# Kernel tuning notes

Measured on AMD Instinct MI355X. Metric: run time of the kernel, lower is better.

## Reference

```python
import jax, jax.numpy as jnp
import numpy as np

SEQ, EMBED, H, QLR, KVLR, RD, VD = 4096, 2048, 16, 512, 512, 64, 128
KD = VD + RD  # full key/query head dim (content + rope)


def _make_rotary_pe(seq_len, dim):
    inv_freq = 1.0 / jnp.power(10000.0, jnp.arange(0, dim, 2) / dim)
    t = jnp.arange(seq_len)
    freqs = jnp.outer(t, inv_freq)  # (seq, dim//2)
    return jnp.sin(freqs), jnp.cos(freqs)


def _apply_rope(x, sin, cos):
    # x: (seq, ..., dim); sin/cos: (seq, dim//2)
    d = x.shape[-1] // 2
    x1, x2 = x[..., :d], x[..., d:]
    sin2 = jnp.concatenate([sin, sin], axis=-1)
    cos2 = jnp.concatenate([cos, cos], axis=-1)
    ne = x.ndim - 2
    sin2 = sin2.reshape(sin2.shape[0], *[1] * ne, sin2.shape[1])
    cos2 = cos2.reshape(cos2.shape[0], *[1] * ne, cos2.shape[1])
    rot = jnp.concatenate([-x2, x1], axis=-1)
    return x * cos2 + rot * sin2


def setup_inputs() -> dict:
    key = jax.random.key(0)
    ks = jax.random.split(key, 8)

    def w(k, out_dim, in_dim):
        return jax.random.normal(k, (out_dim, in_dim), dtype=jnp.float32) * (1.0 / np.sqrt(in_dim))

    x = jax.random.normal(ks[0], (SEQ, EMBED), dtype=jnp.float32)
    mask = jnp.tril(jnp.ones((SEQ, SEQ), dtype=bool))  # causal
    return {
        "x": x,
        "mask": mask,
        "w_q_down": w(ks[1], QLR, EMBED),
        "w_q_up": w(ks[2], H * VD, QLR),
        "w_q_rope": w(ks[3], H * RD, QLR),
        "w_kv_down": w(ks[4], KVLR, EMBED),
        "w_kv_up": w(ks[5], H * 2 * VD, KVLR),
        "w_k_rope": w(ks[6], RD, EMBED),
        "w_out": w(ks[7], EMBED, H * VD),
    }


def reference(x, mask, w_q_down, w_q_up, w_q_rope, w_kv_down, w_kv_up, w_k_rope, w_out):
    seq = x.shape[0]
    # query path through low-rank bottleneck
    c_q = x @ w_q_down.T                                   # (S, QLR)
    q_content = (c_q @ w_q_up.T).reshape(seq, H, VD)       # (S, H, VD)
    q_rope = (c_q @ w_q_rope.T).reshape(seq, H, RD)        # (S, H, RD)
    # kv path through shared low-rank bottleneck
    c_kv = x @ w_kv_down.T                                 # (S, KVLR)
    kv = c_kv @ w_kv_up.T                                  # (S, H*2*VD)
    k_content_flat, v_flat = jnp.split(kv, 2, axis=-1)
    k_content = k_content_flat.reshape(seq, H, VD)
    v = v_flat.reshape(seq, H, VD)
    # shared rope key (one per token, broadcast to heads)
    k_rope_shared = (x @ w_k_rope.T)[:, None, :]           # (S, 1, RD)
    sin, cos = _make_rotary_pe(seq, RD)
    q_rope_rot = _apply_rope(q_rope, sin, cos)             # (S, H, RD)
    k_rope_rot = jnp.tile(_apply_rope(k_rope_shared, sin, cos), (1, H, 1))
    q_final = jnp.concatenate([q_content, q_rope_rot], axis=-1)  # (S, H, KD)
    k_final = jnp.concatenate([k_content, k_rope_rot], axis=-1)  # (S, H, KD)
    # values zero-padded to key dim
    v_padded = jnp.concatenate(
        [v, jnp.zeros((seq, H, RD), dtype=v.dtype)], axis=-1)    # (S, H, KD)
    # scaled dot-product attention per head
    scale = 1.0 / jnp.sqrt(jnp.asarray(KD, dtype=x.dtype))
    scores = jnp.einsum("shd,thd->hst", q_final, k_final) * scale  # (H, S, S)
    scores = jnp.where(mask[None, :, :], scores, jnp.asarray(-1e9, dtype=scores.dtype))
    probs = jax.nn.softmax(scores, axis=-1)
    attn = jnp.einsum("hst,thd->shd", probs, v_padded)             # (S, H, KD)
    attn = attn[..., :VD].reshape(seq, H * VD)                     # drop zero-pad dims
    return attn @ w_out.T                                          # (S, EMBED)
```

## Files before the change

kernel.cpp:

```cpp
#include <hip/hip_runtime.h>


#define SEQ   4096
#define EMBED 2048
#define NHEAD 16
#define QLR   512
#define KVLR  512
#define RD    64
#define VD    128
#define KDIM  192

typedef __attribute__((ext_vector_type(8)))  _Float16 half8;
typedef __attribute__((ext_vector_type(4)))  _Float16 half4;
typedef __attribute__((ext_vector_type(4)))  float    f32x4;
typedef __attribute__((ext_vector_type(16))) float    f32x16;
typedef __attribute__((ext_vector_type(2)))  unsigned int uint2v;
typedef __attribute__((ext_vector_type(4)))  unsigned int uint4v;

__device__ __forceinline__ void gload16(void* lds, const void* g) {
    __builtin_amdgcn_global_load_lds(
        (const __attribute__((address_space(1))) void*)g,
        (__attribute__((address_space(3))) void*)lds, 16, 0, 0);
}

__device__ __forceinline__ unsigned int pkh(float a, float b) {
    auto h = __builtin_amdgcn_cvt_pkrtz(a, b);
    return __builtin_bit_cast(unsigned int, h);
}

__device__ __forceinline__ half8 cvt8(const float* p) {
    const float4 a = *reinterpret_cast<const float4*>(p);
    const float4 b = *reinterpret_cast<const float4*>(p + 4);
    half8 r;
    r[0] = (_Float16)a.x; r[1] = (_Float16)a.y; r[2] = (_Float16)a.z; r[3] = (_Float16)a.w;
    r[4] = (_Float16)b.x; r[5] = (_Float16)b.y; r[6] = (_Float16)b.z; r[7] = (_Float16)b.w;
    return r;
}

__global__ __launch_bounds__(256) void cvt_all(const float* __restrict__ x,
                                               const float* __restrict__ wqd,
                                               const float* __restrict__ wkvd,
                                               const float* __restrict__ wkr,
                                               const float* __restrict__ wqu,
                                               const float* __restrict__ wqr,
                                               const float* __restrict__ wkvu,
                                               _Float16* __restrict__ x_h,
                                               _Float16* __restrict__ wdownh,
                                               _Float16* __restrict__ wquph,
                                               _Float16* __restrict__ wkvuh)
{
    const int b = blockIdx.x;
    if (b < 4096) {
        const int i = b * 256 + threadIdx.x;
        reinterpret_cast<half8*>(x_h)[i] = cvt8(x + i * 8);
    } else if (b < 5248) {
        const int i = (b - 4096) * 256 + threadIdx.x;
        const int e = i * 8, row = e >> 11, col = e & 2047;
        const float* src = row < 512  ? wqd  + (size_t)row * 2048 + col
                         : row < 1024 ? wkvd + (size_t)(row - 512) * 2048 + col
                         : row < 1088 ? wkr  + (size_t)(row - 1024) * 2048 + col
                                      : nullptr;
        half8 r = {};
        if (src) r = cvt8(src);
        reinterpret_cast<half8*>(wdownh)[i] = r;
    } else if (b < 6016) {
        const int i = (b - 5248) * 256 + threadIdx.x;
        const int e = i * 8, row = e >> 9, col = e & 511;
        const float* src = row < 2048 ? wqu + (size_t)row * 512 + col
                                      : wqr + (size_t)(row - 2048) * 512 + col;
        reinterpret_cast<half8*>(wquph)[i] = cvt8(src);
    } else {
        const int i = (b - 6016) * 256 + threadIdx.x;
        reinterpret_cast<half8*>(wkvuh)[i] = cvt8(wkvu + i * 8);
    }
}

__global__ __launch_bounds__(256) void cvt_plain(const float* __restrict__ s,
                                                 _Float16* __restrict__ d, int n8) {
    const int i = blockIdx.x * 256 + threadIdx.x;
    if (i >= n8) return;
    reinterpret_cast<half8*>(d)[i] = cvt8(s + i * 8);
}

template <int EPI>
__global__ __launch_bounds__(256) void gemm_f16(const _Float16* __restrict__ A,
                                                const _Float16* __restrict__ B,
                                                _Float16* __restrict__ o0,
                                                _Float16* __restrict__ o1,
                                                _Float16* __restrict__ o2,
                                                float* __restrict__ of,
                                                int M, int N, int K)
{
    __shared__ _Float16 sA[128 * 64];
    __shared__ _Float16 sB[128 * 64];

    const int tid  = threadIdx.x;
    const int wid  = tid >> 6;
    const int lane = tid & 63;
    const int lr   = lane & 15;
    const int lg   = lane >> 4;
    const int row0 = blockIdx.y * 128;
    const int col0 = blockIdx.x * 128;
    const int war  = (wid >> 1) * 64;
    const int wac  = (wid & 1) * 64;

    const int sr = lane >> 3;
    const int sk = (lane & 7) * 8;
    const _Float16* Ab = A + (size_t)(row0 + wid * 8 + sr) * K + sk;
    const _Float16* Bb = B + (size_t)(col0 + wid * 8 + sr) * K + sk;

    f32x4 acc[4][4] = {};

    for (int k0 = 0; k0 < K; k0 += 64) {
#pragma unroll
        for (int i = 0; i < 4; ++i) {
            const int c = i * 4 + wid;
            gload16((char*)sA + c * 1024, Ab + (size_t)i * 32 * K + k0);
            gload16((char*)sB + c * 1024, Bb + (size_t)i * 32 * K + k0);
        }
        __syncthreads();

#pragma unroll
        for (int kk = 0; kk < 64; kk += 32) {
            half8 a[4], b[4];
#pragma unroll
            for (int i = 0; i < 4; ++i)
                a[i] = *reinterpret_cast<const half8*>(&sA[(war + i * 16 + lr) * 64 + kk + lg * 8]);
#pragma unroll
            for (int j = 0; j < 4; ++j)
                b[j] = *reinterpret_cast<const half8*>(&sB[(wac + j * 16 + lr) * 64 + kk + lg * 8]);
            __builtin_amdgcn_s_setprio(1);
#pragma unroll
            for (int i = 0; i < 4; ++i)
#pragma unroll
                for (int j = 0; j < 4; ++j)
                    acc[i][j] = __builtin_amdgcn_mfma_f32_16x16x32_f16(a[i], b[j], acc[i][j], 0, 0, 0);
            __builtin_amdgcn_s_setprio(0);
        }
        __syncthreads();
    }

#pragma unroll
    for (int i = 0; i < 4; ++i)
#pragma unroll
        for (int j = 0; j < 4; ++j) {
            const int grow0 = row0 + war + i * 16 + lg * 4;
            const int gcol  = col0 + wac + j * 16 + lr;
            if constexpr (EPI == 2) {
                if (gcol >= 2048) {
                    half4 pv;
#pragma unroll
                    for (int r = 0; r < 4; ++r) pv[r] = (_Float16)acc[i][j][r];
                    *reinterpret_cast<half4*>(&o1[(size_t)(gcol - 2048) * SEQ + grow0]) = pv;
                    continue;
                }
            }
#pragma unroll
            for (int r = 0; r < 4; ++r) {
                const int grow = grow0 + r;
                const float v = acc[i][j][r];
                if constexpr (EPI == 0) {
                    if (gcol < 512)       o0[(size_t)grow * 512 + gcol] = (_Float16)v;
                    else if (gcol < 1024) o1[(size_t)grow * 512 + gcol - 512] = (_Float16)v;
                    else if (gcol < 1088) o2[(size_t)grow * 64 + gcol - 1024] = (_Float16)v;
                } else if constexpr (EPI == 1) {
                    if (gcol < 2048)
                        o0[(size_t)grow * (NHEAD * KDIM) + (gcol >> 7) * KDIM + (gcol & 127)] = (_Float16)v;
                    else {
                        const int c = gcol - 2048;
                        o0[(size_t)grow * (NHEAD * KDIM) + (c >> 6) * KDIM + VD + (c & 63)] = (_Float16)v;
                    }
                } else if constexpr (EPI == 2) {
                    o0[((size_t)(gcol >> 7) * SEQ + grow) * KDIM + (gcol & 127)] = (_Float16)v;
                } else {
                    of[(size_t)grow * N + gcol] = v;
                }
            }
        }
}

__global__ __launch_bounds__(256) void rope_kernel(_Float16* __restrict__ qf,
                                                   _Float16* __restrict__ kf,
                                                   const _Float16* __restrict__ ktmp)
{
    __shared__ float s_sin[32], s_cos[32];
    const int s   = blockIdx.x;
    const int tid = threadIdx.x;
    if (tid < 32) {
        const double inv = exp(-(double)tid * (log(10000.0) / 32.0));
        const double ang = (double)s * inv;
        s_sin[tid] = (float)sin(ang);
        s_cos[tid] = (float)cos(ang);
    }
    __syncthreads();

    for (int p = tid; p < NHEAD * 32; p += 256) {
        const int h = p >> 5, i = p & 31;
        const size_t base = (size_t)s * (NHEAD * KDIM) + h * KDIM + VD;
        const float x1 = (float)qf[base + i];
        const float x2 = (float)qf[base + 32 + i];
        const float cs = s_cos[i], sn = s_sin[i];
        qf[base + i]      = (_Float16)(x1 * cs - x2 * sn);
        qf[base + 32 + i] = (_Float16)(x2 * cs + x1 * sn);
    }
    if (tid < 32) {
        const int i = tid;
        const float x1 = (float)ktmp[(size_t)s * RD + i];
        const float x2 = (float)ktmp[(size_t)s * RD + 32 + i];
        const float cs = s_cos[i], sn = s_sin[i];
        const _Float16 r1 = (_Float16)(x1 * cs - x2 * sn);
        const _Float16 r2 = (_Float16)(x2 * cs + x1 * sn);
#pragma unroll
        for (int h = 0; h < NHEAD; ++h) {
            const size_t base = ((size_t)h * SEQ + s) * KDIM + VD;
            kf[base + i]      = r1;
            kf[base + 32 + i] = r2;
        }
    }
}

__global__ __launch_bounds__(256, 2) void fattn(const _Float16* __restrict__ qf,
                                                const _Float16* __restrict__ kf,
                                                const _Float16* __restrict__ vT,
                                                _Float16* __restrict__ attn)
{
    __shared__ _Float16 sK[2][64 * 192];
    __shared__ _Float16 sV[128 * 64];

    const int idx = blockIdx.x;
    const int h   = idx & 15;
    const int j   = idx >> 4;
    const int qt  = (j < 16) ? (31 - 2 * j) : (2 * (j - 16));
    const int q0  = qt * 128;

    const int tid  = threadIdx.x;
    const int wid  = tid >> 6;
    const int lane = tid & 63;
    const int l31  = lane & 31;
    const int h5   = lane >> 5;
    const int x7   = l31 & 7;
    const int qg   = q0 + wid * 32 + l31;
    const int q0w  = q0 + wid * 32;

    const float scale = 0.0721687836487032f;

    const _Float16* ksrc[6];
    int klds[6];
#pragma unroll
    for (int i = 0; i < 6; ++i) {
        const int c   = wid * 6 + i;
        const int gi  = c * 64 + lane;
        const int row = gi / 24;
        const int g   = gi % 24;
        ksrc[i] = kf + ((size_t)h * SEQ + row) * KDIM + ((g ^ (row & 7)) << 3);
        klds[i] = c * 1024;
    }
    const _Float16* vsrc[4];
    int vlds[4];
#pragma unroll
    for (int i = 0; i < 4; ++i) {
        const int c = wid * 4 + i;
        const int d = c * 8 + (lane >> 3);
        vsrc[i] = vT + ((size_t)h * VD + d) * SEQ + (((lane & 7) ^ (lane >> 3)) << 3);
        vlds[i] = c * 1024;
    }

    half8 qfr[12];
    {
        const _Float16* qb_ = qf + (size_t)qg * (NHEAD * KDIM) + h * KDIM + h5 * 8;
#pragma unroll
        for (int ks = 0; ks < 12; ++ks)
            qfr[ks] = *reinterpret_cast<const half8*>(qb_ + ks * 16);
    }

    f32x16 o0 = {}, o1 = {}, o2 = {}, o3 = {};
    float m_ = -1e30f, l_ = 0.0f;

    const int nt = 2 * qt + 2;

#pragma unroll
    for (int i = 0; i < 6; ++i) gload16((char*)sK[0] + klds[i], ksrc[i]);
#pragma unroll
    for (int i = 0; i < 4; ++i) gload16((char*)sV + vlds[i], vsrc[i]);
    __syncthreads();

    int cur = 0;
    for (int t = 0; t < nt; ++t) {
        const int j0 = t * 64;
        const bool more = (t + 1 < nt);

        if (more) {
            const size_t joff = (size_t)(j0 + 64) * KDIM;
#pragma unroll
            for (int i = 0; i < 6; ++i)
                gload16((char*)sK[cur ^ 1] + klds[i], ksrc[i] + joff);
        }

        f32x16 s0 = {}, s1 = {};
        {
            const char* kb = (const char*)sK[cur];
            __builtin_amdgcn_s_setprio(1);
#pragma unroll
            for (int ks = 0; ks < 12; ++ks) {
                const int go = ((ks * 2 + h5) ^ x7) << 4;
                const half8 ka = *reinterpret_cast<const half8*>(kb + l31 * 384 + go);
                const half8 kc = *reinterpret_cast<const half8*>(kb + (32 + l31) * 384 + go);
                s0 = __builtin_amdgcn_mfma_f32_32x32x16_f16(ka, qfr[ks], s0, 0, 0, 0);
                s1 = __builtin_amdgcn_mfma_f32_32x32x16_f16(kc, qfr[ks], s1, 0, 0, 0);
            }
            __builtin_amdgcn_s_setprio(0);
        }

#pragma unroll
        for (int m = 0; m < 16; ++m) { s0[m] *= scale; s1[m] *= scale; }
        if (j0 + 63 > q0w) {
#pragma unroll
            for (int m = 0; m < 16; ++m) {
                const int kv = j0 + (m & 3) + 8 * (m >> 2) + 4 * h5;
                if (kv > qg)      s0[m] = -3.0e38f;
                if (kv + 32 > qg) s1[m] = -3.0e38f;
            }
        }

        float mx = s0[0];
#pragma unroll
        for (int m = 1; m < 16; ++m) mx = fmaxf(mx, s0[m]);
#pragma unroll
        for (int m = 0; m < 16; ++m) mx = fmaxf(mx, s1[m]);
        mx = fmaxf(mx, __shfl_xor(mx, 32, 64));

        if (!__all(mx - m_ <= 8.0f)) {
            const float mn = fmaxf(m_, mx);
            const float alpha = __expf(m_ - mn);
            m_ = mn;
            l_ *= alpha;
#pragma unroll
            for (int m = 0; m < 16; ++m) {
                o0[m] *= alpha; o1[m] *= alpha; o2[m] *= alpha; o3[m] *= alpha;
            }
        }
        float rs = 0.0f;
#pragma unroll
        for (int m = 0; m < 16; ++m) { const float p = __expf(s0[m] - m_); s0[m] = p; rs += p; }
#pragma unroll
        for (int m = 0; m < 16; ++m) { const float p = __expf(s1[m] - m_); s1[m] = p; rs += p; }
        rs += __shfl_xor(rs, 32, 64);
        l_ += rs;

        half8 pb0, pb1, pb2, pb3;
        {
            unsigned int x, x2, y, y2;
            x  = pkh(s0[0], s0[1]);  x2 = pkh(s0[2], s0[3]);
            y  = pkh(s0[4], s0[5]);  y2 = pkh(s0[6], s0[7]);
            uint2v r1 = __builtin_amdgcn_permlane32_swap(x, y, false, false);
            uint2v r2 = __builtin_amdgcn_permlane32_swap(x2, y2, false, false);
            { uint4v u = { r1[0], r2[0], r1[1], r2[1] }; pb0 = __builtin_bit_cast(half8, u); }
            x  = pkh(s0[8], s0[9]);  x2 = pkh(s0[10], s0[11]);
            y  = pkh(s0[12], s0[13]); y2 = pkh(s0[14], s0[15]);
            r1 = __builtin_amdgcn_permlane32_swap(x, y, false, false);
            r2 = __builtin_amdgcn_permlane32_swap(x2, y2, false, false);
            { uint4v u = { r1[0], r2[0], r1[1], r2[1] }; pb1 = __builtin_bit_cast(half8, u); }
            x  = pkh(s1[0], s1[1]);  x2 = pkh(s1[2], s1[3]);
            y  = pkh(s1[4], s1[5]);  y2 = pkh(s1[6], s1[7]);
            r1 = __builtin_amdgcn_permlane32_swap(x, y, false, false);
            r2 = __builtin_amdgcn_permlane32_swap(x2, y2, false, false);
            { uint4v u = { r1[0], r2[0], r1[1], r2[1] }; pb2 = __builtin_bit_cast(half8, u); }
            x  = pkh(s1[8], s1[9]);  x2 = pkh(s1[10], s1[11]);
            y  = pkh(s1[12], s1[13]); y2 = pkh(s1[14], s1[15]);
            r1 = __builtin_amdgcn_permlane32_swap(x, y, false, false);
            r2 = __builtin_amdgcn_permlane32_swap(x2, y2, false, false);
            { uint4v u = { r1[0], r2[0], r1[1], r2[1] }; pb3 = __builtin_bit_cast(half8, u); }
        }

        if (more) asm volatile("s_waitcnt vmcnt(6)" ::: "memory");
        else      asm volatile("s_waitcnt vmcnt(0)" ::: "memory");
        __builtin_amdgcn_sched_barrier(0);
        __builtin_amdgcn_s_barrier();

        {
            const char* vbse = (const char*)sV;
            __builtin_amdgcn_s_setprio(1);
#pragma unroll
            for (int ks = 0; ks < 4; ++ks) {
                const int go = ((ks * 2 + h5) ^ x7) << 4;
                const half8 pbk = ks == 0 ? pb0 : ks == 1 ? pb1 : ks == 2 ? pb2 : pb3;
                const half8 v0 = *reinterpret_cast<const half8*>(vbse + (l31)      * 128 + go);
                const half8 v1 = *reinterpret_cast<const half8*>(vbse + (32 + l31) * 128 + go);
                const half8 v2 = *reinterpret_cast<const half8*>(vbse + (64 + l31) * 128 + go);
                const half8 v3 = *reinterpret_cast<const half8*>(vbse + (96 + l31) * 128 + go);
                o0 = __builtin_amdgcn_mfma_f32_32x32x16_f16(v0, pbk, o0, 0, 0, 0);
                o1 = __builtin_amdgcn_mfma_f32_32x32x16_f16(v1, pbk, o1, 0, 0, 0);
                o2 = __builtin_amdgcn_mfma_f32_32x32x16_f16(v2, pbk, o2, 0, 0, 0);
                o3 = __builtin_amdgcn_mfma_f32_32x32x16_f16(v3, pbk, o3, 0, 0, 0);
            }
            __builtin_amdgcn_s_setprio(0);
        }

        asm volatile("s_waitcnt lgkmcnt(0)" ::: "memory");
        __builtin_amdgcn_sched_barrier(0);
        __builtin_amdgcn_s_barrier();

        if (more) {
            const int jn = j0 + 64;
#pragma unroll
            for (int i = 0; i < 4; ++i)
                gload16((char*)sV + vlds[i], vsrc[i] + jn);
            asm volatile("s_waitcnt vmcnt(4)" ::: "memory");
            __builtin_amdgcn_sched_barrier(0);
            __builtin_amdgcn_s_barrier();
        }
        cur ^= 1;
    }

    const float invl = 1.0f / l_;
    _Float16* ob = attn + (size_t)qg * (NHEAD * VD) + h * VD + 4 * h5;
#pragma unroll
    for (int g = 0; g < 4; ++g) {
#pragma unroll
        for (int pp = 0; pp < 2; ++pp) {
            const int m = g * 4 + pp * 2;
            const int dof = pp * 2 + 8 * g;
            *reinterpret_cast<unsigned int*>(ob + dof) =
                pkh(o0[m] * invl, o0[m + 1] * invl);
            *reinterpret_cast<unsigned int*>(ob + 32 + dof) =
                pkh(o1[m] * invl, o1[m + 1] * invl);
            *reinterpret_cast<unsigned int*>(ob + 64 + dof) =
                pkh(o2[m] * invl, o2[m + 1] * invl);
            *reinterpret_cast<unsigned int*>(ob + 96 + dof) =
                pkh(o3[m] * invl, o3[m + 1] * invl);
        }
    }
}

extern "C" void kernel_launch(void* const* d_in, const int* in_sizes, int n_in,
                              void* d_out, int out_size, void* d_ws, size_t ws_size,
                              hipStream_t stream)
{
    (void)in_sizes; (void)n_in; (void)out_size; (void)ws_size;
    const float* x    = (const float*)d_in[0];
    const float* wqd  = (const float*)d_in[2];
    const float* wqu  = (const float*)d_in[3];
    const float* wqr  = (const float*)d_in[4];
    const float* wkvd = (const float*)d_in[5];
    const float* wkvu = (const float*)d_in[6];
    const float* wkr  = (const float*)d_in[7];
    const float* wout = (const float*)d_in[8];
    float* out = (float*)d_out;

    char* ws = (char*)d_ws;
    _Float16* x_h    = (_Float16*)ws; ws += (size_t)SEQ * EMBED * 2;
    _Float16* wdownh = (_Float16*)ws; ws += (size_t)1152 * EMBED * 2;
    _Float16* wquph  = (_Float16*)ws; ws += (size_t)3072 * QLR * 2;
    _Float16* wkvuh  = (_Float16*)ws; ws += (size_t)4096 * KVLR * 2;
    _Float16* c_q    = (_Float16*)ws; ws += (size_t)SEQ * QLR * 2;
    _Float16* c_kv   = (_Float16*)ws; ws += (size_t)SEQ * KVLR * 2;
    _Float16* ktmp   = (_Float16*)ws; ws += (size_t)SEQ * RD * 2;
    _Float16* qfin   = (_Float16*)ws; ws += (size_t)SEQ * NHEAD * KDIM * 2;
    _Float16* kfin   = (_Float16*)ws; ws += (size_t)SEQ * NHEAD * KDIM * 2;
    _Float16* vT     = (_Float16*)ws; ws += (size_t)NHEAD * VD * SEQ * 2;
    _Float16* attn   = x_h;
    _Float16* wouth  = c_q;

    dim3 blk(256);

    cvt_all<<<dim3(7040), blk, 0, stream>>>(x, wqd, wkvd, wkr, wqu, wqr, wkvu,
                                            x_h, wdownh, wquph, wkvuh);

    gemm_f16<0><<<dim3(9, 32), blk, 0, stream>>>(
        x_h, wdownh, c_q, c_kv, ktmp, nullptr, SEQ, 1152, EMBED);
    gemm_f16<1><<<dim3(24, 32), blk, 0, stream>>>(
        c_q, wquph, qfin, nullptr, nullptr, nullptr, SEQ, 3072, QLR);
    gemm_f16<2><<<dim3(32, 32), blk, 0, stream>>>(
        c_kv, wkvuh, kfin, vT, nullptr, nullptr, SEQ, 4096, KVLR);

    cvt_plain<<<dim3(2048), blk, 0, stream>>>(wout, wouth, EMBED * EMBED / 8);

    rope_kernel<<<dim3(SEQ), blk, 0, stream>>>(qfin, kfin, ktmp);
    fattn<<<dim3(512), blk, 0, stream>>>(qfin, kfin, vT, attn);
    gemm_f16<3><<<dim3(16, 32), blk, 0, stream>>>(
        attn, wouth, nullptr, nullptr, nullptr, out, SEQ, EMBED, NHEAD * VD);
}
```

Before: 332.6 us.

## Drop K double-buffering and raise attention occupancy to four blocks per CU

Shrinks the K tile from a double buffer to a single LDS buffer, cutting LDS per block so four blocks can share a CU, and raises launch bounds to match. The hand-tuned waitcnt/barrier software pipeline is replaced by plain __syncthreads around each tile, with the next K and V loads issued only after compute finishes. Latency hiding moves from intra-block prefetch to inter-block occupancy. The tighter launch bound cuts the per-thread register budget, which risks spilling given the large Q fragment and output accumulators.

```diff
diff --git a/kernel.cpp b/kernel.cpp
--- a/kernel.cpp
+++ b/kernel.cpp
@@ -219,12 +219,12 @@
     }
 }
 
-__global__ __launch_bounds__(256, 2) void fattn(const _Float16* __restrict__ qf,
+__global__ __launch_bounds__(256, 4) void fattn(const _Float16* __restrict__ qf,
                                                 const _Float16* __restrict__ kf,
                                                 const _Float16* __restrict__ vT,
                                                 _Float16* __restrict__ attn)
 {
-    __shared__ _Float16 sK[2][64 * 192];
+    __shared__ _Float16 sK[64 * 192];
     __shared__ _Float16 sV[128 * 64];
 
     const int idx = blockIdx.x;
@@ -279,26 +279,18 @@
     const int nt = 2 * qt + 2;
 
 #pragma unroll
-    for (int i = 0; i < 6; ++i) gload16((char*)sK[0] + klds[i], ksrc[i]);
+    for (int i = 0; i < 6; ++i) gload16((char*)sK + klds[i], ksrc[i]);
 #pragma unroll
     for (int i = 0; i < 4; ++i) gload16((char*)sV + vlds[i], vsrc[i]);
-    __syncthreads();
-
-    int cur = 0;
+
     for (int t = 0; t < nt; ++t) {
         const int j0 = t * 64;
-        const bool more = (t + 1 < nt);
-
-        if (more) {
-            const size_t joff = (size_t)(j0 + 64) * KDIM;
-#pragma unroll
-            for (int i = 0; i < 6; ++i)
-                gload16((char*)sK[cur ^ 1] + klds[i], ksrc[i] + joff);
-        }
+
+        __syncthreads();
 
         f32x16 s0 = {}, s1 = {};
         {
-            const char* kb = (const char*)sK[cur];
+            const char* kb = (const char*)sK;
             __builtin_amdgcn_s_setprio(1);
 #pragma unroll
             for (int ks = 0; ks < 12; ++ks) {
@@ -372,11 +364,6 @@
             { uint4v u = { r1[0], r2[0], r1[1], r2[1] }; pb3 = __builtin_bit_cast(half8, u); }
         }
 
-        if (more) asm volatile("s_waitcnt vmcnt(6)" ::: "memory");
-        else      asm volatile("s_waitcnt vmcnt(0)" ::: "memory");
-        __builtin_amdgcn_sched_barrier(0);
-        __builtin_amdgcn_s_barrier();
-
         {
             const char* vbse = (const char*)sV;
             __builtin_amdgcn_s_setprio(1);
@@ -396,20 +383,15 @@
             __builtin_amdgcn_s_setprio(0);
         }
 
-        asm volatile("s_waitcnt lgkmcnt(0)" ::: "memory");
-        __builtin_amdgcn_sched_barrier(0);
-        __builtin_amdgcn_s_barrier();
-
-        if (more) {
-            const int jn = j0 + 64;
-#pragma unroll
-            for (int i = 0; i < 4; ++i)
-                gload16((char*)sV + vlds[i], vsrc[i] + jn);
-            asm volatile("s_waitcnt vmcnt(4)" ::: "memory");
-            __builtin_amdgcn_sched_barrier(0);
-            __builtin_amdgcn_s_barrier();
-        }
-        cur ^= 1;
+        __syncthreads();
+
+        if (t + 1 < nt) {
+            const size_t joff = (size_t)(j0 + 64) * KDIM;
+#pragma unroll
+            for (int i = 0; i < 6; ++i) gload16((char*)sK + klds[i], ksrc[i] + joff);
+#pragma unroll
+            for (int i = 0; i < 4; ++i) gload16((char*)sV + vlds[i], vsrc[i] + j0 + 64);
+        }
     }
 
     const float invl = 1.0f / l_;
```

Result: slower. 633.0 us (+90.3%).

## Add row-group rotation to K/V LDS swizzle and simplify loop barriers

Applied to the files above, without the earlier changes.

Adds a per-row-group rotation on top of the XOR swizzle for the K and V shared-memory tiles. The rotation is applied both in the global-to-LDS load addresses and in the MFMA operand reads, and is meant to spread accesses across more LDS banks and cut bank conflicts. It also replaces the hand-tuned partial vmcnt/lgkmcnt waits and raw barriers with plain __syncthreads calls, and drops the barrier that followed the V prefetch. The simpler barriers may force a full drain of outstanding global loads, including the next K tile's prefetch, before the PV step. That risks losing load/compute overlap.

```diff
diff --git a/kernel.cpp b/kernel.cpp
--- a/kernel.cpp
+++ b/kernel.cpp
@@ -239,6 +239,8 @@
     const int l31  = lane & 31;
     const int h5   = lane >> 5;
     const int x7   = l31 & 7;
+    const int rotk = 6 * (l31 >> 3);
+    const int rotv = 2 * (l31 >> 3);
     const int qg   = q0 + wid * 32 + l31;
     const int q0w  = q0 + wid * 32;
 
@@ -251,8 +253,10 @@
         const int c   = wid * 6 + i;
         const int gi  = c * 64 + lane;
         const int row = gi / 24;
-        const int g   = gi % 24;
-        ksrc[i] = kf + ((size_t)h * SEQ + row) * KDIM + ((g ^ (row & 7)) << 3);
+        const int p   = gi % 24;
+        const int rot = 6 * ((row >> 3) & 3);
+        const int L   = ((p - rot + 24) % 24) ^ (row & 7);
+        ksrc[i] = kf + ((size_t)h * SEQ + row) * KDIM + (L << 3);
         klds[i] = c * 1024;
     }
     const _Float16* vsrc[4];
@@ -261,7 +265,8 @@
     for (int i = 0; i < 4; ++i) {
         const int c = wid * 4 + i;
         const int d = c * 8 + (lane >> 3);
-        vsrc[i] = vT + ((size_t)h * VD + d) * SEQ + (((lane & 7) ^ (lane >> 3)) << 3);
+        const int L = (((lane & 7) - 2 * (c & 3) + 8) & 7) ^ (lane >> 3);
+        vsrc[i] = vT + ((size_t)h * VD + d) * SEQ + (L << 3);
         vlds[i] = c * 1024;
     }
 
@@ -287,9 +292,8 @@
     int cur = 0;
     for (int t = 0; t < nt; ++t) {
         const int j0 = t * 64;
-        const bool more = (t + 1 < nt);
-
-        if (more) {
+
+        if (t + 1 < nt) {
             const size_t joff = (size_t)(j0 + 64) * KDIM;
 #pragma unroll
             for (int i = 0; i < 6; ++i)
@@ -302,7 +306,9 @@
             __builtin_amdgcn_s_setprio(1);
 #pragma unroll
             for (int ks = 0; ks < 12; ++ks) {
-                const int go = ((ks * 2 + h5) ^ x7) << 4;
+                int pk = ((ks * 2 + h5) ^ x7) + rotk;
+                pk = pk >= 24 ? pk - 24 : pk;
+                const int go = pk << 4;
                 const half8 ka = *reinterpret_cast<const half8*>(kb + l31 * 384 + go);
                 const half8 kc = *reinterpret_cast<const half8*>(kb + (32 + l31) * 384 + go);
                 s0 = __builtin_amdgcn_mfma_f32_32x32x16_f16(ka, qfr[ks], s0, 0, 0, 0);
@@ -372,17 +378,14 @@
             { uint4v u = { r1[0], r2[0], r1[1], r2[1] }; pb3 = __builtin_bit_cast(half8, u); }
         }
 
-        if (more) asm volatile("s_waitcnt vmcnt(6)" ::: "memory");
-        else      asm volatile("s_waitcnt vmcnt(0)" ::: "memory");
-        __builtin_amdgcn_sched_barrier(0);
-        __builtin_amdgcn_s_barrier();
+        __syncthreads();
 
         {
             const char* vbse = (const char*)sV;
             __builtin_amdgcn_s_setprio(1);
 #pragma unroll
             for (int ks = 0; ks < 4; ++ks) {
-                const int go = ((ks * 2 + h5) ^ x7) << 4;
+                const int go = ((((ks * 2 + h5) ^ x7) + rotv) & 7) << 4;
                 const half8 pbk = ks == 0 ? pb0 : ks == 1 ? pb1 : ks == 2 ? pb2 : pb3;
                 const half8 v0 = *reinterpret_cast<const half8*>(vbse + (l31)      * 128 + go);
                 const half8 v1 = *reinterpret_cast<const half8*>(vbse + (32 + l31) * 128 + go);
@@ -396,18 +399,13 @@
             __builtin_amdgcn_s_setprio(0);
         }
 
-        asm volatile("s_waitcnt lgkmcnt(0)" ::: "memory");
-        __builtin_amdgcn_sched_barrier(0);
-        __builtin_amdgcn_s_barrier();
-
-        if (more) {
+        __syncthreads();
+
+        if (t + 1 < nt) {
             const int jn = j0 + 64;
 #pragma unroll
             for (int i = 0; i < 4; ++i)
                 gload16((char*)sV + vlds[i], vsrc[i] + jn);
-            asm volatile("s_waitcnt vmcnt(4)" ::: "memory");
-            __builtin_amdgcn_sched_barrier(0);
-            __builtin_amdgcn_s_barrier();
         }
         cur ^= 1;
     }
```

Measured after the change: 337.2 us. Within noise of the previous version (+1.4%).
